# Kernel optimization log

Hardware: AMD Instinct MI355X
Metric: run time of the kernel (lower is better)

The kernel has to match this reference:

```python
import jax, jax.numpy as jnp
import numpy as np

N_USERS = 8192
D = 128
E = 262144        # known edges (nonzero_idx rows)
K = 131072        # static pad size for data-dependent candidate extraction
COS_THR = 0.3
TAU = 0.2


def setup_inputs() -> dict:
    key = jax.random.key(0)
    k1, k2, k3, k4 = jax.random.split(key, 4)
    user_emb = jax.random.normal(k1, (N_USERS, D), dtype=jnp.float32)
    nonzero_idx = jax.random.randint(k2, (E, 2), 0, N_USERS)
    W = jax.random.normal(k3, (2, 2 * D), dtype=jnp.float32) * 0.05  # mlp_s weight [2, 2*latent]
    b = jnp.zeros((2,), dtype=jnp.float32)                            # mlp_s bias
    gumbel_noise = jax.random.gumbel(k4, (E + K, 2), dtype=jnp.float32)
    return {"user_emb": user_emb, "W": W, "b": b,
            "gumbel_noise": gumbel_noise, "nonzero_idx": nonzero_idx}


def reference(user_emb, W, b, gumbel_noise, nonzero_idx):
    n = user_emb.shape[0]
    # ---- get_candidate_pair ----
    norm = jnp.linalg.norm(user_emb, axis=1, keepdims=True)
    u = user_emb / jnp.maximum(norm, 1e-12)          # F.normalize(dim=1)
    cos = u @ u.T                                    # [n, n]
    diag = jnp.arange(n)
    cos = cos.at[diag, diag].set(-1.0)               # fill_diagonal_(-1)
    cos = cos.at[nonzero_idx[:, 0], nonzero_idx[:, 1]].set(-1.0)
    mask = cos > COS_THR
    # static-size nonzero; padded slots point at (0,0) where cos == -1,
    # so they behave as invalid candidates (weight 0 downstream).
    ci, cj = jnp.nonzero(mask, size=K, fill_value=0)
    cand_vals = cos[ci, cj]                          # padded entries = -1
    cand_idx = jnp.stack([ci, cj], axis=1)           # [K, 2]

    # ---- forward ----
    pair_idx = jnp.concatenate([nonzero_idx, cand_idx], axis=0)   # [E+K, 2]
    u_emb = user_emb[pair_idx[:, 0]]
    v_emb = user_emb[pair_idx[:, 1]]
    concat_emb = jnp.concatenate([u_emb, v_emb], axis=1)          # [E+K, 2D]
    logits = concat_emb @ W.T + b                                 # [E+K, 2]

    # hard gumbel-softmax (straight-through)
    y_soft = jax.nn.softmax((logits + gumbel_noise) / TAU, axis=-1)
    y_hard = jax.nn.one_hot(jnp.argmax(y_soft, axis=-1), 2, dtype=y_soft.dtype)
    gumbel_output = y_hard + y_soft - jax.lax.stop_gradient(y_soft)
    gumbel_retain = gumbel_output[:, 0]                           # [E+K]

    # ---- get_edge_weight ----
    cand_w = jnp.maximum(cand_vals, 0.0)                          # masked_fill(<0, 0)
    weights = jnp.concatenate([jnp.ones((E,), dtype=cand_w.dtype), cand_w])
    w = gumbel_retain * weights                                   # [E+K]
    gumbel_01 = w
    gumbel_retain_w = jnp.concatenate([w[:, None], w[:, None]], axis=0)  # [2(E+K), 1]
    return gumbel_01, gumbel_retain_w, pair_idx
```

## Files before the change

### kernel.cpp

```cpp
#include <hip/hip_runtime.h>
#include <hip/hip_bf16.h>
#include <math.h>

#define N_USERS 8192
#define DIMS    128
#define EDGES   262144
#define KCAND   131072
#define NTOT    (EDGES + KCAND)
#define LISTCAP 131072
#define CAPB    512
#define NTILES  2080
#define COS_THR 0.3f
#define EPS_SEL 6e-3f
#define LOGIT_MARGIN 2e-3f
#define DEADKEY 0xFFFFFFFFu

typedef short bf16x8 __attribute__((ext_vector_type(8)));
typedef float f32x4  __attribute__((ext_vector_type(4)));


__global__ __launch_bounds__(256) void prep_k(const float* __restrict__ x,
                                              const float* __restrict__ W,
                                              const int* __restrict__ nz,
                                              float* __restrict__ un,
                                              unsigned short* __restrict__ u0,
                                              float4* __restrict__ P,
                                              unsigned* __restrict__ excl) {
  if (blockIdx.x < 32) {
#pragma clang fp contract(off)
    int i = blockIdx.x * 256 + threadIdx.x;
    const float* r = x + (size_t)i * DIMS;
    float a[8];
#pragma unroll
    for (int j = 0; j < 8; ++j) { float t = r[j]; a[j] = t * t; }
    for (int b8 = 8; b8 < DIMS; b8 += 8) {
#pragma unroll
      for (int j = 0; j < 8; ++j) { float t = r[b8 + j]; a[j] = a[j] + t * t; }
    }
    float s = ((a[0] + a[1]) + (a[2] + a[3])) + ((a[4] + a[5]) + (a[6] + a[7]));
    float n = (float)sqrt((double)s);
    n = fmaxf(n, 1e-12f);
    unsigned short* slab = u0 + (size_t)(i >> 7) * 16384 + (i & 127) * 8;
#pragma unroll
    for (int cq = 0; cq < 16; ++cq) {
      unsigned short tmp[8];
#pragma unroll
      for (int t = 0; t < 8; ++t) {
        float v = r[cq * 8 + t] / n;
        un[(size_t)i * DIMS + cq * 8 + t] = v;
        __hip_bfloat16 h = __float2bfloat16(v);
        tmp[t] = *(unsigned short*)&h;
      }
      *(uint4*)(slab + (size_t)cq * 1024) = *(uint4*)tmp;
    }
    float a0 = 0.f, b0 = 0.f, a1 = 0.f, b1 = 0.f;
    for (int k = 0; k < DIMS; ++k) {
      float t = r[k];
      a0 = fmaf(t, W[k], a0);
      b0 = fmaf(t, W[128 + k], b0);
      a1 = fmaf(t, W[256 + k], a1);
      b1 = fmaf(t, W[384 + k], b1);
    }
    P[i] = make_float4(a0, b0, a1, b1);
  } else {
    int t = (blockIdx.x - 32) * 256 + threadIdx.x;
    if (t < EDGES) {
      int i = nz[2 * t], j = nz[2 * t + 1];
      atomicOr(&excl[(size_t)i * 256 + (j >> 5)], 1u << (j & 31));
    }
  }
}

__global__ __launch_bounds__(512) void mfma_pass(const unsigned short* __restrict__ u0,
                                                 uint2* __restrict__ list,
                                                 int* __restrict__ gcount) {
  __shared__ __align__(16) unsigned short As[4][4][128][8];
  __shared__ __align__(16) unsigned short Bs[4][4][128][8];
  __shared__ uint2 svec[CAPB];
  __shared__ int lcnt, lbase;

  const int tid  = threadIdx.x;
  const int lane = tid & 63;
  const int wv   = tid >> 6;
  const int quad = lane >> 4;
  const int l15  = lane & 15;

  int rem = blockIdx.x, bi = 0;
  while (rem >= 64 - bi) { rem -= 64 - bi; ++bi; }
  const int bj = bi + rem;
  const int I0 = bi * 128, J0 = bj * 128;
  const int moff = (wv & 3) * 32, noff = (wv >> 2) * 64;

  if (tid == 0) lcnt = 0;

  const uint4* __restrict__ Aslab = (const uint4*)(u0 + (size_t)bi * 16384);
  const uint4* __restrict__ Bslab = (const uint4*)(u0 + (size_t)bj * 16384);
  uint4 pA[4], pB[4];
#pragma unroll
  for (int it = 0; it < 4; ++it) {
    pA[it] = Aslab[it * 512 + tid];
    pB[it] = Bslab[it * 512 + tid];
  }
#pragma unroll
  for (int it = 0; it < 4; ++it) {
    ((uint4*)As)[it * 512 + tid] = pA[it];
    ((uint4*)Bs)[it * 512 + tid] = pB[it];
  }
  __syncthreads();

  f32x4 acc[2][4];
#pragma unroll
  for (int mt = 0; mt < 2; ++mt)
#pragma unroll
    for (int nt = 0; nt < 4; ++nt)
#pragma unroll
      for (int g = 0; g < 4; ++g) acc[mt][nt][g] = 0.f;

#pragma unroll
  for (int kc = 0; kc < 4; ++kc) {
    bf16x8 af[2], bfr[4];
#pragma unroll
    for (int mt = 0; mt < 2; ++mt)
      af[mt] = *(const bf16x8*)&As[kc][quad][moff + mt * 16 + l15][0];
#pragma unroll
    for (int nt = 0; nt < 4; ++nt)
      bfr[nt] = *(const bf16x8*)&Bs[kc][quad][noff + nt * 16 + l15][0];
#pragma unroll
    for (int mt = 0; mt < 2; ++mt)
#pragma unroll
      for (int nt = 0; nt < 4; ++nt)
        acc[mt][nt] = __builtin_amdgcn_mfma_f32_16x16x32_bf16(
            af[mt], bfr[nt], acc[mt][nt], 0, 0, 0);
  }

#pragma unroll
  for (int mt = 0; mt < 2; ++mt)
#pragma unroll
    for (int nt = 0; nt < 4; ++nt)
#pragma unroll
      for (int g = 0; g < 4; ++g) {
        float v = acc[mt][nt][g];
        if (v > COS_THR - EPS_SEL) {
          int i = I0 + moff + mt * 16 + quad * 4 + g;
          int j = J0 + noff + nt * 16 + l15;
          if (j > i) {
            int idx = atomicAdd(&lcnt, 2);
            if (idx + 1 < CAPB) {
              svec[idx]     = make_uint2(((unsigned)i << 13) | j,
                                         __float_as_uint(v));
              svec[idx + 1] = make_uint2(((unsigned)j << 13) | i,
                                         __float_as_uint(v));
            }
          }
        }
      }

  __syncthreads();
  int n = min(lcnt, CAPB);
  if (tid == 0) lbase = atomicAdd(gcount, n);
  __syncthreads();
  int base = lbase;
  for (int t = tid; t < n; t += 512) {
    int o = base + t;
    if (o < LISTCAP) list[o] = svec[t];
  }
}

__global__ __launch_bounds__(256) void resolve_hist_k(const float* __restrict__ un,
                                                      const unsigned* __restrict__ excl,
                                                      uint2* __restrict__ list,
                                                      const int* __restrict__ gcount,
                                                      int* __restrict__ row_cnt) {
  int t = blockIdx.x * 256 + threadIdx.x;
  int n = min(*gcount, LISTCAP);
  if (t >= n) return;
  uint2 e = list[t];
  int i = e.x >> 13, j = e.x & 8191;
  unsigned word = excl[(size_t)i * 256 + (j >> 5)];
  bool alive = !(i == j || ((word >> (j & 31)) & 1u));
  float v = __uint_as_float(e.y);
  if (alive && v <= COS_THR + EPS_SEL) {
    const float* a = un + (size_t)i * DIMS;
    const float* b = un + (size_t)j * DIMS;
    float s = 0.f;
    for (int k = 0; k < DIMS; ++k) s = fmaf(a[k], b[k], s);
    alive = (s > COS_THR);
    if (alive) list[t] = make_uint2(e.x, __float_as_uint(s));
  }
  if (!alive) list[t] = make_uint2(DEADKEY, 0u);
  else        atomicAdd(&row_cnt[i], 1);
}

__global__ __launch_bounds__(256) void scan8k(const int* __restrict__ cnt,
                                              int* __restrict__ off) {
  __shared__ int sm[256];
  int t = threadIdx.x;
  int base = t * 32;
  int s = 0;
  for (int i = 0; i < 32; ++i) s += cnt[base + i];
  sm[t] = s;
  __syncthreads();
  int x = s;
  for (int d = 1; d < 256; d <<= 1) {
    int y = (t >= d) ? sm[t - d] : 0;
    __syncthreads();
    x += y;
    sm[t] = x;
    __syncthreads();
  }
  int run = x - s;
  for (int i = 0; i < 32; ++i) { off[base + i] = run; run += cnt[base + i]; }
  if (t == 255) off[N_USERS] = x;
}

__global__ __launch_bounds__(256) void scatter_pad_k(const uint2* __restrict__ list,
                                                     const int* __restrict__ gcount,
                                                     const int* __restrict__ row_off,
                                                     int* __restrict__ row_pos,
                                                     int* __restrict__ cand_i,
                                                     int* __restrict__ cand_j,
                                                     float* __restrict__ cand_v) {
  int t = blockIdx.x * 256 + threadIdx.x;
  int n = min(*gcount, LISTCAP);
  int M = row_off[N_USERS];
  if (t < n) {
    uint2 e = list[t];
    if (e.x != DEADKEY) {
      int i = e.x >> 13, j = e.x & 8191;
      int pos = row_off[i] + atomicAdd(&row_pos[i], 1);
      if (pos < KCAND) {
        cand_i[pos] = i;
        cand_j[pos] = j;
        cand_v[pos] = __uint_as_float(e.y);
      }
    }
  }
  if (t >= M && t < KCAND) { cand_i[t] = 0; cand_j[t] = 0; cand_v[t] = -1.0f; }
}

__global__ __launch_bounds__(256) void sortrow_k(const int* __restrict__ row_off,
                                                 const int* __restrict__ row_cnt,
                                                 int* __restrict__ cand_j,
                                                 float* __restrict__ cand_v) {
  int r = blockIdx.x * 256 + threadIdx.x;
  if (r >= N_USERS) return;
  int o = row_off[r], c = row_cnt[r];
  if (o + c > KCAND) c = max(0, KCAND - o);
  for (int a = 1; a < c; ++a) {
    int jv = cand_j[o + a];
    float vv = cand_v[o + a];
    int b = a - 1;
    while (b >= 0 && cand_j[o + b] > jv) {
      cand_j[o + b + 1] = cand_j[o + b];
      cand_v[o + b + 1] = cand_v[o + b];
      --b;
    }
    cand_j[o + b + 1] = jv;
    cand_v[o + b + 1] = vv;
  }
}

__global__ __launch_bounds__(256) void finalize_k(const float* __restrict__ ue,
                                                  const float* __restrict__ W,
                                                  const float* __restrict__ b,
                                                  const float* __restrict__ g,
                                                  const int* __restrict__ nz,
                                                  const int* __restrict__ cand_i,
                                                  const int* __restrict__ cand_j,
                                                  const float* __restrict__ cand_v,
                                                  const float4* __restrict__ P,
                                                  float* __restrict__ out) {
  int p = blockIdx.x * 256 + threadIdx.x;
  if (p >= NTOT) return;

  int i, j;
  float wgt;
  if (p < EDGES) {
    i = nz[2 * p];
    j = nz[2 * p + 1];
    wgt = 1.0f;
  } else {
    int q = p - EDGES;
    i = cand_i[q];
    j = cand_j[q];
    wgt = fmaxf(cand_v[q], 0.0f);
  }

  float4 Pi = P[i], Pj = P[j];
  float l0 = Pi.x + Pj.y + b[0];
  float l1 = Pi.z + Pj.w + b[1];
  float g0 = g[2 * p], g1 = g[2 * p + 1];
  float s0 = l0 + g0, s1 = l1 + g1;

  if (fabsf(s0 - s1) < LOGIT_MARGIN) {
    const float* ri = ue + (size_t)i * DIMS;
    const float* rj = ue + (size_t)j * DIMS;
    float e0 = 0.f, e1 = 0.f;
    for (int k = 0; k < DIMS; ++k) {
      e0 = fmaf(ri[k], W[k], e0);
      e1 = fmaf(ri[k], W[256 + k], e1);
    }
    for (int k = 0; k < DIMS; ++k) {
      e0 = fmaf(rj[k], W[128 + k], e0);
      e1 = fmaf(rj[k], W[384 + k], e1);
    }
    s0 = (e0 + b[0]) + g0;
    s1 = (e1 + b[1]) + g1;
  }

  float w = (s0 >= s1) ? wgt : 0.0f;

  out[p] = w;
  out[NTOT + p] = w;
  out[2 * NTOT + p] = w;
  out[3 * NTOT + 2 * p + 0] = (float)i;
  out[3 * NTOT + 2 * p + 1] = (float)j;
}

extern "C" void kernel_launch(void* const* d_in, const int* in_sizes, int n_in,
                              void* d_out, int out_size, void* d_ws, size_t ws_size,
                              hipStream_t stream) {
  (void)in_sizes; (void)n_in; (void)out_size; (void)ws_size;

  const float* user_emb = (const float*)d_in[0];
  const float* W        = (const float*)d_in[1];
  const float* b        = (const float*)d_in[2];
  const float* gnoise   = (const float*)d_in[3];
  const int*   nz       = (const int*)d_in[4];
  float* out = (float*)d_out;

  char* ws = (char*)d_ws;
  float*          un      = (float*)(ws + 0);
  unsigned short* u0      = (unsigned short*)(ws + (4u << 20));
  unsigned*       excl    = (unsigned*)(ws + (6u << 20));
  char*           zbase   = ws + (14u << 20);
  int*            gcount  = (int*)(zbase);
  int*            row_cnt = (int*)(zbase + 64);
  int*            row_pos = (int*)(zbase + 64 + 32768);
  int*            row_off = (int*)(ws + (14u << 20) + (96u << 10));
  uint2*          list    = (uint2*)(ws + (15u << 20));
  int*            cand_i  = (int*)(ws + (16u << 20));
  int*            cand_j  = (int*)(ws + (16u << 20) + (512u << 10));
  float*          cand_v  = (float*)(ws + (17u << 20));
  float4*         P       = (float4*)(ws + (17u << 20) + (512u << 10));

  hipMemsetAsync(excl, 0, (8u << 20) + (96u << 10), stream);

  prep_k<<<32 + EDGES / 256, 256, 0, stream>>>(user_emb, W, nz, un, u0, P, excl);
  mfma_pass<<<NTILES, 512, 0, stream>>>(u0, list, gcount);
  resolve_hist_k<<<LISTCAP / 256, 256, 0, stream>>>(un, excl, list, gcount,
                                                    row_cnt);
  scan8k<<<1, 256, 0, stream>>>(row_cnt, row_off);
  scatter_pad_k<<<KCAND / 256, 256, 0, stream>>>(list, gcount, row_off, row_pos,
                                                 cand_i, cand_j, cand_v);
  sortrow_k<<<N_USERS / 256, 256, 0, stream>>>(row_off, row_cnt, cand_j, cand_v);
  finalize_k<<<NTOT / 256, 256, 0, stream>>>(user_emb, W, b, gnoise, nz,
                                             cand_i, cand_j, cand_v, P, out);
}
```

Baseline: 161.1 us.

## Fuse post-MFMA stages into one cooperative kernel with grid syncs

Merges five post-processing kernels (resolve/histogram, scan, scatter, row sort, finalize) into a single cooperative persistent kernel with 512 blocks separated by grid.sync barriers. This removes the per-launch overhead and the gaps between small kernels. Padding slots are now written directly in finalize instead of going through the cand arrays. It risks slower grid-wide barriers, lower parallelism in the grid-stride loops, and a single-block scan that leaves the rest of the grid idle.

```diff
diff --git a/kernel.cpp b/kernel.cpp
--- a/kernel.cpp
+++ b/kernel.cpp
@@ -1,6 +1,9 @@
 #include <hip/hip_runtime.h>
 #include <hip/hip_bf16.h>
+#include <hip/hip_cooperative_groups.h>
 #include <math.h>
+
+namespace cg = cooperative_groups;
 
 #define N_USERS 8192
 #define DIMS    128
@@ -14,6 +17,9 @@
 #define EPS_SEL 6e-3f
 #define LOGIT_MARGIN 2e-3f
 #define DEADKEY 0xFFFFFFFFu
+
+#define POST_BLOCKS 512
+#define POST_GSZ    (POST_BLOCKS * 256)
 
 typedef short bf16x8 __attribute__((ext_vector_type(8)));
 typedef float f32x4  __attribute__((ext_vector_type(4)));
@@ -166,64 +172,72 @@
   }
 }
 
-__global__ __launch_bounds__(256) void resolve_hist_k(const float* __restrict__ un,
-                                                      const unsigned* __restrict__ excl,
-                                                      uint2* __restrict__ list,
-                                                      const int* __restrict__ gcount,
-                                                      int* __restrict__ row_cnt) {
-  int t = blockIdx.x * 256 + threadIdx.x;
-  int n = min(*gcount, LISTCAP);
-  if (t >= n) return;
-  uint2 e = list[t];
-  int i = e.x >> 13, j = e.x & 8191;
-  unsigned word = excl[(size_t)i * 256 + (j >> 5)];
-  bool alive = !(i == j || ((word >> (j & 31)) & 1u));
-  float v = __uint_as_float(e.y);
-  if (alive && v <= COS_THR + EPS_SEL) {
-    const float* a = un + (size_t)i * DIMS;
-    const float* b = un + (size_t)j * DIMS;
-    float s = 0.f;
-    for (int k = 0; k < DIMS; ++k) s = fmaf(a[k], b[k], s);
-    alive = (s > COS_THR);
-    if (alive) list[t] = make_uint2(e.x, __float_as_uint(s));
-  }
-  if (!alive) list[t] = make_uint2(DEADKEY, 0u);
-  else        atomicAdd(&row_cnt[i], 1);
-}
-
-__global__ __launch_bounds__(256) void scan8k(const int* __restrict__ cnt,
-                                              int* __restrict__ off) {
+__global__ __launch_bounds__(256) void post_k(const float* __restrict__ un,
+                                              const unsigned* __restrict__ excl,
+                                              uint2* __restrict__ list,
+                                              const int* __restrict__ gcount,
+                                              int* __restrict__ row_cnt,
+                                              int* __restrict__ row_off,
+                                              int* __restrict__ row_pos,
+                                              int* __restrict__ cand_i,
+                                              int* __restrict__ cand_j,
+                                              float* __restrict__ cand_v,
+                                              const float* __restrict__ ue,
+                                              const float* __restrict__ W,
+                                              const float* __restrict__ b,
+                                              const float* __restrict__ g,
+                                              const int* __restrict__ nz,
+                                              const float4* __restrict__ P,
+                                              float* __restrict__ out) {
+  cg::grid_group grid = cg::this_grid();
+  const int gtid = blockIdx.x * 256 + threadIdx.x;
+
+  const int n = min(*gcount, LISTCAP);
+  for (int t = gtid; t < n; t += POST_GSZ) {
+    uint2 e = list[t];
+    int i = e.x >> 13, j = e.x & 8191;
+    unsigned word = excl[(size_t)i * 256 + (j >> 5)];
+    bool alive = !(i == j || ((word >> (j & 31)) & 1u));
+    float v = __uint_as_float(e.y);
+    if (alive && v <= COS_THR + EPS_SEL) {
+      const float* a = un + (size_t)i * DIMS;
+      const float* bb = un + (size_t)j * DIMS;
+      float s = 0.f;
+      for (int k = 0; k < DIMS; ++k) s = fmaf(a[k], bb[k], s);
+      alive = (s > COS_THR);
+      if (alive) list[t] = make_uint2(e.x, __float_as_uint(s));
+    }
+    if (!alive) list[t] = make_uint2(DEADKEY, 0u);
+    else        atomicAdd(&row_cnt[i], 1);
+  }
+  grid.sync();
+
   __shared__ int sm[256];
-  int t = threadIdx.x;
-  int base = t * 32;
-  int s = 0;
-  for (int i = 0; i < 32; ++i) s += cnt[base + i];
-  sm[t] = s;
-  __syncthreads();
-  int x = s;
-  for (int d = 1; d < 256; d <<= 1) {
-    int y = (t >= d) ? sm[t - d] : 0;
+  if (blockIdx.x == 0) {
+    int t = threadIdx.x;
+    int base = t * 32;
+    int s = 0;
+    for (int i2 = 0; i2 < 32; ++i2) s += row_cnt[base + i2];
+    sm[t] = s;
     __syncthreads();
-    x += y;
-    sm[t] = x;
-    __syncthreads();
-  }
-  int run = x - s;
-  for (int i = 0; i < 32; ++i) { off[base + i] = run; run += cnt[base + i]; }
-  if (t == 255) off[N_USERS] = x;
-}
-
-__global__ __launch_bounds__(256) void scatter_pad_k(const uint2* __restrict__ list,
-                                                     const int* __restrict__ gcount,
-                                                     const int* __restrict__ row_off,
-                                                     int* __restrict__ row_pos,
-                                                     int* __restrict__ cand_i,
-                                                     int* __restrict__ cand_j,
-                                                     float* __restrict__ cand_v) {
-  int t = blockIdx.x * 256 + threadIdx.x;
-  int n = min(*gcount, LISTCAP);
-  int M = row_off[N_USERS];
-  if (t < n) {
+    int x = s;
+    for (int d = 1; d < 256; d <<= 1) {
+      int y = (t >= d) ? sm[t - d] : 0;
+      __syncthreads();
+      x += y;
+      sm[t] = x;
+      __syncthreads();
+    }
+    int run = x - s;
+    for (int i2 = 0; i2 < 32; ++i2) {
+      row_off[base + i2] = run;
+      run += row_cnt[base + i2];
+    }
+    if (t == 255) row_off[N_USERS] = x;
+  }
+  grid.sync();
+
+  for (int t = gtid; t < n; t += POST_GSZ) {
     uint2 e = list[t];
     if (e.x != DEADKEY) {
       int i = e.x >> 13, j = e.x & 8191;
@@ -235,86 +249,79 @@
       }
     }
   }
-  if (t >= M && t < KCAND) { cand_i[t] = 0; cand_j[t] = 0; cand_v[t] = -1.0f; }
-}
-
-__global__ __launch_bounds__(256) void sortrow_k(const int* __restrict__ row_off,
-                                                 const int* __restrict__ row_cnt,
-                                                 int* __restrict__ cand_j,
-                                                 float* __restrict__ cand_v) {
-  int r = blockIdx.x * 256 + threadIdx.x;
-  if (r >= N_USERS) return;
-  int o = row_off[r], c = row_cnt[r];
-  if (o + c > KCAND) c = max(0, KCAND - o);
-  for (int a = 1; a < c; ++a) {
-    int jv = cand_j[o + a];
-    float vv = cand_v[o + a];
-    int b = a - 1;
-    while (b >= 0 && cand_j[o + b] > jv) {
-      cand_j[o + b + 1] = cand_j[o + b];
-      cand_v[o + b + 1] = cand_v[o + b];
-      --b;
-    }
-    cand_j[o + b + 1] = jv;
-    cand_v[o + b + 1] = vv;
-  }
-}
-
-__global__ __launch_bounds__(256) void finalize_k(const float* __restrict__ ue,
-                                                  const float* __restrict__ W,
-                                                  const float* __restrict__ b,
-                                                  const float* __restrict__ g,
-                                                  const int* __restrict__ nz,
-                                                  const int* __restrict__ cand_i,
-                                                  const int* __restrict__ cand_j,
-                                                  const float* __restrict__ cand_v,
-                                                  const float4* __restrict__ P,
-                                                  float* __restrict__ out) {
-  int p = blockIdx.x * 256 + threadIdx.x;
-  if (p >= NTOT) return;
-
-  int i, j;
-  float wgt;
-  if (p < EDGES) {
-    i = nz[2 * p];
-    j = nz[2 * p + 1];
-    wgt = 1.0f;
-  } else {
-    int q = p - EDGES;
-    i = cand_i[q];
-    j = cand_j[q];
-    wgt = fmaxf(cand_v[q], 0.0f);
-  }
-
-  float4 Pi = P[i], Pj = P[j];
-  float l0 = Pi.x + Pj.y + b[0];
-  float l1 = Pi.z + Pj.w + b[1];
-  float g0 = g[2 * p], g1 = g[2 * p + 1];
-  float s0 = l0 + g0, s1 = l1 + g1;
-
-  if (fabsf(s0 - s1) < LOGIT_MARGIN) {
-    const float* ri = ue + (size_t)i * DIMS;
-    const float* rj = ue + (size_t)j * DIMS;
-    float e0 = 0.f, e1 = 0.f;
-    for (int k = 0; k < DIMS; ++k) {
-      e0 = fmaf(ri[k], W[k], e0);
-      e1 = fmaf(ri[k], W[256 + k], e1);
-    }
-    for (int k = 0; k < DIMS; ++k) {
-      e0 = fmaf(rj[k], W[128 + k], e0);
-      e1 = fmaf(rj[k], W[384 + k], e1);
-    }
-    s0 = (e0 + b[0]) + g0;
-    s1 = (e1 + b[1]) + g1;
-  }
-
-  float w = (s0 >= s1) ? wgt : 0.0f;
-
-  out[p] = w;
-  out[NTOT + p] = w;
-  out[2 * NTOT + p] = w;
-  out[3 * NTOT + 2 * p + 0] = (float)i;
-  out[3 * NTOT + 2 * p + 1] = (float)j;
+  grid.sync();
+
+  for (int r = gtid; r < N_USERS; r += POST_GSZ) {
+    int o = row_off[r], c = row_cnt[r];
+    if (o + c > KCAND) c = max(0, KCAND - o);
+    for (int a = 1; a < c; ++a) {
+      int jv = cand_j[o + a];
+      float vv = cand_v[o + a];
+      int bq = a - 1;
+      while (bq >= 0 && cand_j[o + bq] > jv) {
+        cand_j[o + bq + 1] = cand_j[o + bq];
+        cand_v[o + bq + 1] = cand_v[o + bq];
+        --bq;
+      }
+      cand_j[o + bq + 1] = jv;
+      cand_v[o + bq + 1] = vv;
+    }
+  }
+  grid.sync();
+
+  const int M = row_off[N_USERS];
+  for (int p = gtid; p < NTOT; p += POST_GSZ) {
+    int i, j;
+    float wgt;
+    if (p < EDGES) {
+      i = nz[2 * p];
+      j = nz[2 * p + 1];
+      wgt = 1.0f;
+    } else {
+      int q = p - EDGES;
+      if (q >= M) {
+        out[p] = 0.0f;
+        out[NTOT + p] = 0.0f;
+        out[2 * NTOT + p] = 0.0f;
+        out[3 * NTOT + 2 * p + 0] = 0.0f;
+        out[3 * NTOT + 2 * p + 1] = 0.0f;
+        continue;
+      }
+      i = cand_i[q];
+      j = cand_j[q];
+      wgt = fmaxf(cand_v[q], 0.0f);
+    }
+
+    float4 Pi = P[i], Pj = P[j];
+    float l0 = Pi.x + Pj.y + b[0];
+    float l1 = Pi.z + Pj.w + b[1];
+    float g0 = g[2 * p], g1 = g[2 * p + 1];
+    float s0 = l0 + g0, s1 = l1 + g1;
+
+    if (fabsf(s0 - s1) < LOGIT_MARGIN) {
+      const float* ri = ue + (size_t)i * DIMS;
+      const float* rj = ue + (size_t)j * DIMS;
+      float e0 = 0.f, e1 = 0.f;
+      for (int k = 0; k < DIMS; ++k) {
+        e0 = fmaf(ri[k], W[k], e0);
+        e1 = fmaf(ri[k], W[256 + k], e1);
+      }
+      for (int k = 0; k < DIMS; ++k) {
+        e0 = fmaf(rj[k], W[128 + k], e0);
+        e1 = fmaf(rj[k], W[384 + k], e1);
+      }
+      s0 = (e0 + b[0]) + g0;
+      s1 = (e1 + b[1]) + g1;
+    }
+
+    float w = (s0 >= s1) ? wgt : 0.0f;
+
+    out[p] = w;
+    out[NTOT + p] = w;
+    out[2 * NTOT + p] = w;
+    out[3 * NTOT + 2 * p + 0] = (float)i;
+    out[3 * NTOT + 2 * p + 1] = (float)j;
+  }
 }
 
 extern "C" void kernel_launch(void* const* d_in, const int* in_sizes, int n_in,
@@ -348,12 +355,27 @@
 
   prep_k<<<32 + EDGES / 256, 256, 0, stream>>>(user_emb, W, nz, un, u0, P, excl);
   mfma_pass<<<NTILES, 512, 0, stream>>>(u0, list, gcount);
-  resolve_hist_k<<<LISTCAP / 256, 256, 0, stream>>>(un, excl, list, gcount,
-                                                    row_cnt);
-  scan8k<<<1, 256, 0, stream>>>(row_cnt, row_off);
-  scatter_pad_k<<<KCAND / 256, 256, 0, stream>>>(list, gcount, row_off, row_pos,
-                                                 cand_i, cand_j, cand_v);
-  sortrow_k<<<N_USERS / 256, 256, 0, stream>>>(row_off, row_cnt, cand_j, cand_v);
-  finalize_k<<<NTOT / 256, 256, 0, stream>>>(user_emb, W, b, gnoise, nz,
-                                             cand_i, cand_j, cand_v, P, out);
+
+  const float* un_c   = un;
+  const unsigned* excl_c = excl;
+  uint2* list_c       = list;
+  const int* gcount_c = gcount;
+  int* row_cnt_c      = row_cnt;
+  int* row_off_c      = row_off;
+  int* row_pos_c      = row_pos;
+  int* cand_i_c       = cand_i;
+  int* cand_j_c       = cand_j;
+  float* cand_v_c     = cand_v;
+  const float* ue_c   = user_emb;
+  const float* W_c    = W;
+  const float* b_c    = b;
+  const float* g_c    = gnoise;
+  const int* nz_c     = nz;
+  const float4* P_c   = P;
+  float* out_c        = out;
+  void* args[] = {&un_c, &excl_c, &list_c, &gcount_c, &row_cnt_c, &row_off_c,
+                  &row_pos_c, &cand_i_c, &cand_j_c, &cand_v_c, &ue_c, &W_c,
+                  &b_c, &g_c, &nz_c, &P_c, &out_c};
+  hipLaunchCooperativeKernel((void*)post_k, dim3(POST_BLOCKS), dim3(256),
+                             args, 0, stream);
 }
```

Measured after the change: 372.3 us. +131.1%, slower.

## Fuse candidate resolution into MFMA pass and parallelize row prep

Applied to the files above, without the earlier changes.

Fuses the resolve/histogram kernel into the MFMA tile epilogue: borderline cosines are recomputed in fp32, exclusions are checked per direction, and row counts are accumulated right there, so only live candidates reach the list. This removes one launch and a full list read/write pass. Padding is moved from the scatter kernel into finalize, which writes zeros for slots past the live count. The prep kernel now uses 8 threads per row with shuffle reductions instead of one serial thread per row. The trade-off is divergent fp32 dot products and global atomics inside the MFMA epilogue.

```diff
diff --git a/kernel.cpp b/kernel.cpp
--- a/kernel.cpp
+++ b/kernel.cpp
@@ -13,7 +13,6 @@
 #define COS_THR 0.3f
 #define EPS_SEL 6e-3f
 #define LOGIT_MARGIN 2e-3f
-#define DEADKEY 0xFFFFFFFFu
 
 typedef short bf16x8 __attribute__((ext_vector_type(8)));
 typedef float f32x4  __attribute__((ext_vector_type(4)));
@@ -26,44 +25,53 @@
                                               unsigned short* __restrict__ u0,
                                               float4* __restrict__ P,
                                               unsigned* __restrict__ excl) {
-  if (blockIdx.x < 32) {
+  if (blockIdx.x < 256) {
 #pragma clang fp contract(off)
-    int i = blockIdx.x * 256 + threadIdx.x;
+    const int tid  = threadIdx.x;
+    const int rloc = tid >> 3;
+    const int j    = tid & 7;
+    const int i    = blockIdx.x * 32 + rloc;
     const float* r = x + (size_t)i * DIMS;
-    float a[8];
-#pragma unroll
-    for (int j = 0; j < 8; ++j) { float t = r[j]; a[j] = t * t; }
-    for (int b8 = 8; b8 < DIMS; b8 += 8) {
-#pragma unroll
-      for (int j = 0; j < 8; ++j) { float t = r[b8 + j]; a[j] = a[j] + t * t; }
-    }
-    float s = ((a[0] + a[1]) + (a[2] + a[3])) + ((a[4] + a[5]) + (a[6] + a[7]));
+
+    float vals[16];
+    float a = 0.f;
+#pragma unroll
+    for (int b8 = 0; b8 < 16; ++b8) {
+      float t = r[b8 * 8 + j];
+      vals[b8] = t;
+      a = a + t * t;
+    }
+    a = a + __shfl_xor(a, 1, 64);
+    a = a + __shfl_xor(a, 2, 64);
+    float s = a + __shfl_xor(a, 4, 64);
     float n = (float)sqrt((double)s);
     n = fmaxf(n, 1e-12f);
+
     unsigned short* slab = u0 + (size_t)(i >> 7) * 16384 + (i & 127) * 8;
-#pragma unroll
-    for (int cq = 0; cq < 16; ++cq) {
-      unsigned short tmp[8];
-#pragma unroll
-      for (int t = 0; t < 8; ++t) {
-        float v = r[cq * 8 + t] / n;
-        un[(size_t)i * DIMS + cq * 8 + t] = v;
-        __hip_bfloat16 h = __float2bfloat16(v);
-        tmp[t] = *(unsigned short*)&h;
-      }
-      *(uint4*)(slab + (size_t)cq * 1024) = *(uint4*)tmp;
-    }
-    float a0 = 0.f, b0 = 0.f, a1 = 0.f, b1 = 0.f;
-    for (int k = 0; k < DIMS; ++k) {
-      float t = r[k];
-      a0 = fmaf(t, W[k], a0);
-      b0 = fmaf(t, W[128 + k], b0);
-      a1 = fmaf(t, W[256 + k], a1);
-      b1 = fmaf(t, W[384 + k], b1);
-    }
-    P[i] = make_float4(a0, b0, a1, b1);
+    float p0 = 0.f, p1 = 0.f, p2 = 0.f, p3 = 0.f;
+#pragma unroll
+    for (int b8 = 0; b8 < 16; ++b8) {
+      int k = b8 * 8 + j;
+      float t = vals[b8];
+      float v = t / n;
+      un[(size_t)i * DIMS + k] = v;
+      __hip_bfloat16 h = __float2bfloat16(v);
+      slab[(size_t)b8 * 1024 + j] = *(unsigned short*)&h;
+      p0 = fmaf(t, W[k], p0);
+      p1 = fmaf(t, W[128 + k], p1);
+      p2 = fmaf(t, W[256 + k], p2);
+      p3 = fmaf(t, W[384 + k], p3);
+    }
+#pragma unroll
+    for (int m = 1; m < 8; m <<= 1) {
+      p0 += __shfl_xor(p0, m, 64);
+      p1 += __shfl_xor(p1, m, 64);
+      p2 += __shfl_xor(p2, m, 64);
+      p3 += __shfl_xor(p3, m, 64);
+    }
+    if (j == 0) P[i] = make_float4(p0, p1, p2, p3);
   } else {
-    int t = (blockIdx.x - 32) * 256 + threadIdx.x;
+    int t = (blockIdx.x - 256) * 256 + threadIdx.x;
     if (t < EDGES) {
       int i = nz[2 * t], j = nz[2 * t + 1];
       atomicOr(&excl[(size_t)i * 256 + (j >> 5)], 1u << (j & 31));
@@ -72,8 +80,11 @@
 }
 
 __global__ __launch_bounds__(512) void mfma_pass(const unsigned short* __restrict__ u0,
+                                                 const float* __restrict__ un,
+                                                 const unsigned* __restrict__ excl,
                                                  uint2* __restrict__ list,
-                                                 int* __restrict__ gcount) {
+                                                 int* __restrict__ gcount,
+                                                 int* __restrict__ row_cnt) {
   __shared__ __align__(16) unsigned short As[4][4][128][8];
   __shared__ __align__(16) unsigned short Bs[4][4][128][8];
   __shared__ uint2 svec[CAPB];
@@ -144,12 +155,34 @@
           int i = I0 + moff + mt * 16 + quad * 4 + g;
           int j = J0 + noff + nt * 16 + l15;
           if (j > i) {
-            int idx = atomicAdd(&lcnt, 2);
-            if (idx + 1 < CAPB) {
-              svec[idx]     = make_uint2(((unsigned)i << 13) | j,
-                                         __float_as_uint(v));
-              svec[idx + 1] = make_uint2(((unsigned)j << 13) | i,
-                                         __float_as_uint(v));
+            float vv = v;
+            bool pass = true;
+            if (v <= COS_THR + EPS_SEL) {
+              const float* a = un + (size_t)i * DIMS;
+              const float* bb = un + (size_t)j * DIMS;
+              float s2 = 0.f;
+              for (int k = 0; k < DIMS; ++k) s2 = fmaf(a[k], bb[k], s2);
+              pass = (s2 > COS_THR);
+              vv = s2;
+            }
+            if (pass) {
+              unsigned wij = excl[(size_t)i * 256 + (j >> 5)];
+              unsigned wji = excl[(size_t)j * 256 + (i >> 5)];
+              unsigned uvv = __float_as_uint(vv);
+              if (!((wij >> (j & 31)) & 1u)) {
+                int idx = atomicAdd(&lcnt, 1);
+                if (idx < CAPB) {
+                  svec[idx] = make_uint2(((unsigned)i << 13) | j, uvv);
+                  atomicAdd(&row_cnt[i], 1);
+                }
+              }
+              if (!((wji >> (i & 31)) & 1u)) {
+                int idx = atomicAdd(&lcnt, 1);
+                if (idx < CAPB) {
+                  svec[idx] = make_uint2(((unsigned)j << 13) | i, uvv);
+                  atomicAdd(&row_cnt[j], 1);
+                }
+              }
             }
           }
         }
@@ -164,31 +197,6 @@
     int o = base + t;
     if (o < LISTCAP) list[o] = svec[t];
   }
-}
-
-__global__ __launch_bounds__(256) void resolve_hist_k(const float* __restrict__ un,
-                                                      const unsigned* __restrict__ excl,
-                                                      uint2* __restrict__ list,
-                                                      const int* __restrict__ gcount,
-                                                      int* __restrict__ row_cnt) {
-  int t = blockIdx.x * 256 + threadIdx.x;
-  int n = min(*gcount, LISTCAP);
-  if (t >= n) return;
-  uint2 e = list[t];
-  int i = e.x >> 13, j = e.x & 8191;
-  unsigned word = excl[(size_t)i * 256 + (j >> 5)];
-  bool alive = !(i == j || ((word >> (j & 31)) & 1u));
-  float v = __uint_as_float(e.y);
-  if (alive && v <= COS_THR + EPS_SEL) {
-    const float* a = un + (size_t)i * DIMS;
-    const float* b = un + (size_t)j * DIMS;
-    float s = 0.f;
-    for (int k = 0; k < DIMS; ++k) s = fmaf(a[k], b[k], s);
-    alive = (s > COS_THR);
-    if (alive) list[t] = make_uint2(e.x, __float_as_uint(s));
-  }
-  if (!alive) list[t] = make_uint2(DEADKEY, 0u);
-  else        atomicAdd(&row_cnt[i], 1);
 }
 
 __global__ __launch_bounds__(256) void scan8k(const int* __restrict__ cnt,
@@ -213,29 +221,24 @@
   if (t == 255) off[N_USERS] = x;
 }
 
-__global__ __launch_bounds__(256) void scatter_pad_k(const uint2* __restrict__ list,
-                                                     const int* __restrict__ gcount,
-                                                     const int* __restrict__ row_off,
-                                                     int* __restrict__ row_pos,
-                                                     int* __restrict__ cand_i,
-                                                     int* __restrict__ cand_j,
-                                                     float* __restrict__ cand_v) {
+__global__ __launch_bounds__(256) void scatter_k(const uint2* __restrict__ list,
+                                                 const int* __restrict__ gcount,
+                                                 const int* __restrict__ row_off,
+                                                 int* __restrict__ row_pos,
+                                                 int* __restrict__ cand_i,
+                                                 int* __restrict__ cand_j,
+                                                 float* __restrict__ cand_v) {
   int t = blockIdx.x * 256 + threadIdx.x;
   int n = min(*gcount, LISTCAP);
-  int M = row_off[N_USERS];
-  if (t < n) {
-    uint2 e = list[t];
-    if (e.x != DEADKEY) {
-      int i = e.x >> 13, j = e.x & 8191;
-      int pos = row_off[i] + atomicAdd(&row_pos[i], 1);
-      if (pos < KCAND) {
-        cand_i[pos] = i;
-        cand_j[pos] = j;
-        cand_v[pos] = __uint_as_float(e.y);
-      }
-    }
-  }
-  if (t >= M && t < KCAND) { cand_i[t] = 0; cand_j[t] = 0; cand_v[t] = -1.0f; }
+  if (t >= n) return;
+  uint2 e = list[t];
+  int i = e.x >> 13, j = e.x & 8191;
+  int pos = row_off[i] + atomicAdd(&row_pos[i], 1);
+  if (pos < KCAND) {
+    cand_i[pos] = i;
+    cand_j[pos] = j;
+    cand_v[pos] = __uint_as_float(e.y);
+  }
 }
 
 __global__ __launch_bounds__(256) void sortrow_k(const int* __restrict__ row_off,
@@ -268,6 +271,7 @@
                                                   const int* __restrict__ cand_i,
                                                   const int* __restrict__ cand_j,
                                                   const float* __restrict__ cand_v,
+                                                  const int* __restrict__ row_off,
                                                   const float4* __restrict__ P,
                                                   float* __restrict__ out) {
   int p = blockIdx.x * 256 + threadIdx.x;
@@ -281,6 +285,14 @@
     wgt = 1.0f;
   } else {
     int q = p - EDGES;
+    if (q >= row_off[N_USERS]) {
+      out[p] = 0.0f;
+      out[NTOT + p] = 0.0f;
+      out[2 * NTOT + p] = 0.0f;
+      out[3 * NTOT + 2 * p + 0] = 0.0f;
+      out[3 * NTOT + 2 * p + 1] = 0.0f;
+      return;
+    }
     i = cand_i[q];
     j = cand_j[q];
     wgt = fmaxf(cand_v[q], 0.0f);
@@ -346,14 +358,13 @@
 
   hipMemsetAsync(excl, 0, (8u << 20) + (96u << 10), stream);
 
-  prep_k<<<32 + EDGES / 256, 256, 0, stream>>>(user_emb, W, nz, un, u0, P, excl);
-  mfma_pass<<<NTILES, 512, 0, stream>>>(u0, list, gcount);
-  resolve_hist_k<<<LISTCAP / 256, 256, 0, stream>>>(un, excl, list, gcount,
-                                                    row_cnt);
+  prep_k<<<256 + EDGES / 256, 256, 0, stream>>>(user_emb, W, nz, un, u0, P, excl);
+  mfma_pass<<<NTILES, 512, 0, stream>>>(u0, un, excl, list, gcount, row_cnt);
   scan8k<<<1, 256, 0, stream>>>(row_cnt, row_off);
-  scatter_pad_k<<<KCAND / 256, 256, 0, stream>>>(list, gcount, row_off, row_pos,
-                                                 cand_i, cand_j, cand_v);
+  scatter_k<<<LISTCAP / 256, 256, 0, stream>>>(list, gcount, row_off, row_pos,
+                                               cand_i, cand_j, cand_v);
   sortrow_k<<<N_USERS / 256, 256, 0, stream>>>(row_off, row_cnt, cand_j, cand_v);
   finalize_k<<<NTOT / 256, 256, 0, stream>>>(user_emb, W, b, gnoise, nz,
-                                             cand_i, cand_j, cand_v, P, out);
-}
+                                             cand_i, cand_j, cand_v, row_off,
+                                             P, out);
+}
```

After: 151.7 us. 1.06x faster.
